# Kernel optimization log

Measured on AMD Instinct MI355X. Metric: run time of the kernel, lower is better.

The kernel has to match this reference:

```python
import jax, jax.numpy as jnp
import numpy as np

N = 40000
E = 640000
IN_C = 128
HID = 256
HEADS = 8


def _gat(x, W, att_src, att_dst, bias, src, dst, num_nodes, heads, concat):
    # x: [N, Fin], W: [Fin, heads*C], att_*: [heads, C], bias: [out_dim]
    xp = (x @ W).reshape(num_nodes, heads, -1)          # [N, H, C]
    a_s = jnp.sum(xp * att_src, axis=-1)                # [N, H]
    a_d = jnp.sum(xp * att_dst, axis=-1)                # [N, H]
    e = jax.nn.leaky_relu(a_s[src] + a_d[dst], 0.2)     # [E, H]
    # per-destination-node softmax over incoming edges (self-loops guarantee >=1)
    m = jax.ops.segment_max(e, dst, num_segments=num_nodes)
    m = jnp.where(jnp.isfinite(m), m, 0.0)
    ex = jnp.exp(e - m[dst])
    denom = jax.ops.segment_sum(ex, dst, num_segments=num_nodes)
    alpha = ex / (denom[dst] + 1e-16)                   # [E, H]
    out = jax.ops.segment_sum(xp[src] * alpha[..., None], dst, num_segments=num_nodes)  # [N,H,C]
    out = out.reshape(num_nodes, -1) if concat else out.mean(axis=1)
    return out + bias


def setup_inputs() -> dict:
    key = jax.random.key(0)
    ks = jax.random.split(key, 16)
    C = HID // HEADS
    s = 0.05
    return {
        "x": jax.random.normal(ks[0], (N, IN_C), jnp.float32),
        "edge_index": jax.random.randint(ks[1], (2, E), 0, N, jnp.int32),
        "W0": jax.random.normal(ks[2], (IN_C, HEADS * C), jnp.float32) * s,
        "att_s0": jax.random.normal(ks[3], (HEADS, C), jnp.float32) * s,
        "att_d0": jax.random.normal(ks[4], (HEADS, C), jnp.float32) * s,
        "b0": jnp.zeros((HID,), jnp.float32),
        # BatchNorm(256)
        "gamma0": jnp.ones((HID,), jnp.float32),
        "beta0": jnp.zeros((HID,), jnp.float32),
        # skip projection Linear(128 -> 256)
        "W_skip": jax.random.normal(ks[5], (IN_C, HID), jnp.float32) * s,
        "b_skip": jnp.zeros((HID,), jnp.float32),
        # last layer: GATConv(256 -> 256, heads=1, concat=False)
        "W1": jax.random.normal(ks[6], (HID, HID), jnp.float32) * s,
        "att_s1": jax.random.normal(ks[7], (1, HID), jnp.float32) * s,
        "att_d1": jax.random.normal(ks[8], (1, HID), jnp.float32) * s,
        "b1": jnp.zeros((HID,), jnp.float32),
    }


def reference(x, edge_index, W0, att_s0, att_d0, b0, gamma0, beta0,
              W_skip, b_skip, W1, att_s1, att_d1, b1):
    loops = jnp.arange(N, dtype=edge_index.dtype)
    src = jnp.concatenate([edge_index[0], loops])
    dst = jnp.concatenate([edge_index[1], loops])
    # conv 0 (heads=8, concat)
    h = _gat(x, W0, att_s0, att_d0, b0, src, dst, N, HEADS, True)
    # BatchNorm (training-style batch stats, biased variance, eps=1e-5)
    mu = h.mean(axis=0)
    var = h.var(axis=0)
    h = (h - mu) / jnp.sqrt(var + 1e-5) * gamma0 + beta0
    h = jax.nn.elu(h)
    # dropout is identity in eval mode
    # residual: shapes differ (128 vs 256) -> skip_proj(x_initial) + h at i==0
    h = h + (x @ W_skip + b_skip)
    # conv 1 (heads=1, concat=False -> mean over single head)
    out = _gat(h, W1, att_s1, att_d1, b1, src, dst, N, 1, False)
    return out
```

## Files before the change

kernel.cpp:

```cpp
#include <hip/hip_runtime.h>
#include <hip/hip_bf16.h>

#define NN 40000
#define EE 640000
#define ET 680000
#define MPAD 40064
#define LOG2E 1.4426950408889634f

typedef __attribute__((ext_vector_type(8))) short short8;
typedef __attribute__((ext_vector_type(4))) float f32x4;

__device__ __forceinline__ float bf2f(unsigned u) {
    return __uint_as_float(u << 16);
}
__device__ __forceinline__ unsigned short f2bf(float f) {
    unsigned u = __float_as_uint(f);
    return (unsigned short)((u + 0x7FFFu + ((u >> 16) & 1u)) >> 16);
}
__device__ __forceinline__ unsigned pack2(float lo, float hi) {
    return ((unsigned)f2bf(lo)) | (((unsigned)f2bf(hi)) << 16);
}
__device__ __forceinline__ void unpack2(unsigned u, float& lo, float& hi) {
    lo = __uint_as_float(u << 16);
    hi = __uint_as_float(u & 0xffff0000u);
}

__global__ __launch_bounds__(256) void conv_x(const float* __restrict__ x,
                                              unsigned short* __restrict__ xb)
{
    int i = blockIdx.x * 256 + threadIdx.x;
    if (i >= MPAD * 128 / 4) return;
    int row = (i * 4) >> 7;
    ushort4 o;
    if (row < NN) {
        float4 v = ((const float4*)x)[i];
        o.x = f2bf(v.x); o.y = f2bf(v.y); o.z = f2bf(v.z); o.w = f2bf(v.w);
    } else { o.x = o.y = o.z = o.w = 0; }
    ((ushort4*)xb)[i] = o;
}

__global__ __launch_bounds__(256) void conv_wt(const float* __restrict__ W,
                                               unsigned short* __restrict__ Wt, int K)
{
    int i = blockIdx.x * 256 + threadIdx.x;
    if (i >= K * 256) return;
    int c = i / K, k = i - c * K;
    Wt[i] = f2bf(W[(size_t)k * 256 + c]);
}

__global__ __launch_bounds__(256) void gemm_bf16(
    const unsigned short* __restrict__ A, const unsigned short* __restrict__ Btc,
    unsigned short* __restrict__ C0, unsigned short* __restrict__ C1, int K)
{
    __shared__ unsigned short As[128 * 64];
    int tid = threadIdx.x;
    int rb = blockIdx.x * 128, cb = blockIdx.y * 128;
    int lane = tid & 63, wid = tid >> 6;
    int wm = (wid >> 1) * 64, wn = (wid & 1) * 64;
    int lr = lane & 15, lk = lane >> 4;
    f32x4 acc[4][4] = {};
    for (int kb = 0; kb < K; kb += 64) {
        #pragma unroll
        for (int i = 0; i < 4; i++) {
            int flat = tid + i * 256;
            int r = flat >> 3, c8 = flat & 7;
            int4 v = *(const int4*)(A + (size_t)(rb + r) * K + kb + c8 * 8);
            *(int4*)(&As[r * 64 + ((c8 ^ (r & 7)) * 8)]) = v;
        }
        __syncthreads();
        #pragma unroll
        for (int kk = 0; kk < 2; kk++) {
            int kbase = kb + kk * 32 + lk * 8;
            short8 bfr[4], afr[4];
            #pragma unroll
            for (int n = 0; n < 4; n++)
                bfr[n] = *(const short8*)(Btc + (size_t)(cb + wn + n * 16 + lr) * K + kbase);
            #pragma unroll
            for (int m = 0; m < 4; m++) {
                int row = wm + m * 16 + lr;
                int kchunk = kk * 4 + lk;
                afr[m] = *(const short8*)(&As[row * 64 + ((kchunk ^ (row & 7)) * 8)]);
            }
            #pragma unroll
            for (int m = 0; m < 4; m++)
                #pragma unroll
                for (int n = 0; n < 4; n++)
                    acc[m][n] = __builtin_amdgcn_mfma_f32_16x16x32_bf16(afr[m], bfr[n], acc[m][n], 0, 0, 0);
        }
        __syncthreads();
    }
    unsigned short* C = (cb < 256) ? C0 : C1;
    int cbase = cb & 255;
    #pragma unroll
    for (int m = 0; m < 4; m++)
        #pragma unroll
        for (int n = 0; n < 4; n++) {
            int col = cbase + wn + n * 16 + lr;
            #pragma unroll
            for (int j = 0; j < 4; j++) {
                int row = rb + wm + m * 16 + lk * 4 + j;
                C[(size_t)row * 256 + col] = f2bf(acc[m][n][j]);
            }
        }
}

__global__ __launch_bounds__(256) void csr_count(const int* __restrict__ ei, int* __restrict__ deg)
{
    int e = blockIdx.x * blockDim.x + threadIdx.x;
    if (e >= ET) return;
    int d = (e < EE) ? ei[EE + e] : (e - EE);
    atomicAdd(&deg[d], 1);
}

__global__ __launch_bounds__(1024) void exscan(
    const int* __restrict__ deg, int* __restrict__ rowptr, int* __restrict__ cursor)
{
    __shared__ int wsum[16];
    __shared__ int carry_s;
    int tid = threadIdx.x, lane = tid & 63, wid = tid >> 6;
    if (tid == 0) carry_s = 0;
    __syncthreads();
    for (int base = 0; base < NN; base += 1024) {
        int i = base + tid;
        int v = (i < NN) ? deg[i] : 0;
        int sc = v;
        #pragma unroll
        for (int off = 1; off < 64; off <<= 1) {
            int t = __shfl_up(sc, off);
            if (lane >= off) sc += t;
        }
        if (lane == 63) wsum[wid] = sc;
        __syncthreads();
        if (wid == 0 && lane < 16) {
            int t = wsum[lane];
            #pragma unroll
            for (int off = 1; off < 16; off <<= 1) {
                int u = __shfl_up(t, off);
                if (lane >= off) t += u;
            }
            wsum[lane] = t;
        }
        __syncthreads();
        int carry = carry_s;
        int wpre = wid ? wsum[wid - 1] : 0;
        int excl = carry + wpre + sc - v;
        if (i < NN) { rowptr[i] = excl; cursor[i] = excl; }
        __syncthreads();
        if (tid == 0) carry_s = carry + wsum[15];
    }
    if (tid == 0) rowptr[NN] = carry_s;
}

__global__ __launch_bounds__(256) void csr_fill(
    const int* __restrict__ ei, int* __restrict__ cursor, int* __restrict__ adj)
{
    int e = blockIdx.x * blockDim.x + threadIdx.x;
    if (e >= ET) return;
    int s, d;
    if (e < EE) { s = ei[e]; d = ei[EE + e]; } else { s = d = e - EE; }
    int pos = atomicAdd(&cursor[d], 1);
    adj[pos] = s;
}

__global__ __launch_bounds__(256) void attn_node0(
    const unsigned short* __restrict__ xp, const float* __restrict__ att_s,
    const float* __restrict__ att_d, float* __restrict__ a_s, float* __restrict__ a_d)
{
    int t = blockIdx.x * 256 + threadIdx.x;
    if (t >= NN * 8) return;
    int n = t >> 3, h = t & 7;
    const unsigned short* p = xp + (size_t)n * 256 + h * 32;
    float s = 0.f, dd = 0.f;
    #pragma unroll
    for (int i0 = 0; i0 < 32; i0 += 8) {
        uint4 raw = *(const uint4*)(p + i0);
        unsigned vals[4] = {raw.x, raw.y, raw.z, raw.w};
        #pragma unroll
        for (int q = 0; q < 4; q++) {
            float lo, hi;
            unpack2(vals[q], lo, hi);
            s  += lo * att_s[h * 32 + i0 + q * 2] + hi * att_s[h * 32 + i0 + q * 2 + 1];
            dd += lo * att_d[h * 32 + i0 + q * 2] + hi * att_d[h * 32 + i0 + q * 2 + 1];
        }
    }
    a_s[t] = s * LOG2E; a_d[t] = dd * LOG2E;
}

__global__ __launch_bounds__(256) void attn_node1(
    const unsigned short* __restrict__ xp, const float* __restrict__ att_s,
    const float* __restrict__ att_d, float* __restrict__ a_s, float* __restrict__ a_d)
{
    int w = (blockIdx.x * 256 + threadIdx.x) >> 6;
    int lane = threadIdx.x & 63;
    if (w >= NN) return;
    ushort4 raw = ((const ushort4*)(xp + (size_t)w * 256))[lane];
    float4 a = ((const float4*)att_s)[lane];
    float4 b = ((const float4*)att_d)[lane];
    float v0 = bf2f(raw.x), v1 = bf2f(raw.y), v2 = bf2f(raw.z), v3 = bf2f(raw.w);
    float s  = v0 * a.x + v1 * a.y + v2 * a.z + v3 * a.w;
    float dd = v0 * b.x + v1 * b.y + v2 * b.z + v3 * b.w;
    #pragma unroll
    for (int off = 32; off; off >>= 1) {
        s  += __shfl_down(s, off);
        dd += __shfl_down(dd, off);
    }
    if (lane == 0) { a_s[w] = s * LOG2E; a_d[w] = dd * LOG2E; }
}

__global__ __launch_bounds__(256) void gather0(
    const int* __restrict__ adj, const int* __restrict__ rowptr,
    const unsigned short* __restrict__ xp, const float* __restrict__ a_s,
    const float* __restrict__ a_d, unsigned short* __restrict__ out0)
{
    int w = (blockIdx.x * 256 + threadIdx.x) >> 6;
    int lane = threadIdx.x & 63;
    if (w >= NN) return;
    int hl = lane & 31;
    int hw = lane >> 5;
    int h = hl >> 2;
    float ad = a_d[w * 8 + h];
    int p = rowptr[w], end = rowptr[w + 1];
    unsigned loff = (unsigned)hl * 16u;
    float a0=0,a1=0,a2=0,a3=0,a4=0,a5=0,a6=0,a7=0;
    float b0=0,b1=0,b2=0,b3=0,b4=0,b5=0,b6=0,b7=0;
    float den0 = 0.f, den1 = 0.f;
    for (; p + 4 <= end; p += 4) {
        int sA = adj[p + hw];
        int sB = adj[p + 2 + hw];
        float eA = a_s[sA * 8 + h] + ad;
        float eB = a_s[sB * 8 + h] + ad;
        float wA = __builtin_amdgcn_exp2f(fmaxf(eA, 0.2f * eA));
        float wB = __builtin_amdgcn_exp2f(fmaxf(eB, 0.2f * eB));
        uint4 rA = *(const uint4*)((const char*)xp + ((unsigned)sA * 512u + loff));
        uint4 rB = *(const uint4*)((const char*)xp + ((unsigned)sB * 512u + loff));
        den0 += wA; den1 += wB;
        float lo, hi;
        unpack2(rA.x, lo, hi); a0 += wA * lo; a1 += wA * hi;
        unpack2(rA.y, lo, hi); a2 += wA * lo; a3 += wA * hi;
        unpack2(rA.z, lo, hi); a4 += wA * lo; a5 += wA * hi;
        unpack2(rA.w, lo, hi); a6 += wA * lo; a7 += wA * hi;
        unpack2(rB.x, lo, hi); b0 += wB * lo; b1 += wB * hi;
        unpack2(rB.y, lo, hi); b2 += wB * lo; b3 += wB * hi;
        unpack2(rB.z, lo, hi); b4 += wB * lo; b5 += wB * hi;
        unpack2(rB.w, lo, hi); b6 += wB * lo; b7 += wB * hi;
    }
    for (; p + 2 <= end; p += 2) {
        int sA = adj[p + hw];
        float eA = a_s[sA * 8 + h] + ad;
        float wA = __builtin_amdgcn_exp2f(fmaxf(eA, 0.2f * eA));
        uint4 rA = *(const uint4*)((const char*)xp + ((unsigned)sA * 512u + loff));
        den0 += wA;
        float lo, hi;
        unpack2(rA.x, lo, hi); a0 += wA * lo; a1 += wA * hi;
        unpack2(rA.y, lo, hi); a2 += wA * lo; a3 += wA * hi;
        unpack2(rA.z, lo, hi); a4 += wA * lo; a5 += wA * hi;
        unpack2(rA.w, lo, hi); a6 += wA * lo; a7 += wA * hi;
    }
    if (p < end) {
        int sA = adj[p];
        float eA = a_s[sA * 8 + h] + ad;
        float wA = hw ? 0.f : __builtin_amdgcn_exp2f(fmaxf(eA, 0.2f * eA));
        uint4 rA = *(const uint4*)((const char*)xp + ((unsigned)sA * 512u + loff));
        den0 += wA;
        float lo, hi;
        unpack2(rA.x, lo, hi); a0 += wA * lo; a1 += wA * hi;
        unpack2(rA.y, lo, hi); a2 += wA * lo; a3 += wA * hi;
        unpack2(rA.z, lo, hi); a4 += wA * lo; a5 += wA * hi;
        unpack2(rA.w, lo, hi); a6 += wA * lo; a7 += wA * hi;
    }
    a0 += b0; a1 += b1; a2 += b2; a3 += b3;
    a4 += b4; a5 += b5; a6 += b6; a7 += b7;
    float den = den0 + den1;
    den += __shfl_xor(den, 32);
    a0 += __shfl_xor(a0, 32); a1 += __shfl_xor(a1, 32);
    a2 += __shfl_xor(a2, 32); a3 += __shfl_xor(a3, 32);
    a4 += __shfl_xor(a4, 32); a5 += __shfl_xor(a5, 32);
    a6 += __shfl_xor(a6, 32); a7 += __shfl_xor(a7, 32);
    if (hw == 0) {
        float inv = 1.f / (den + 1e-16f);
        uint4 o;
        o.x = pack2(a0 * inv, a1 * inv);
        o.y = pack2(a2 * inv, a3 * inv);
        o.z = pack2(a4 * inv, a5 * inv);
        o.w = pack2(a6 * inv, a7 * inv);
        *(uint4*)((char*)out0 + ((size_t)w * 512u + loff)) = o;
    }
}

__global__ __launch_bounds__(256) void bn_stats(
    const unsigned short* __restrict__ H, float* __restrict__ bnsum, float* __restrict__ bnsq)
{
    int c = threadIdx.x;
    int r0 = blockIdx.x * 64;
    float s = 0.f, sq = 0.f;
    for (int r = r0; r < r0 + 64; r++) {
        float v = bf2f(H[(size_t)r * 256 + c]);
        s += v; sq += v * v;
    }
    atomicAdd(&bnsum[c], s);
    atomicAdd(&bnsq[c], sq);
}

__global__ __launch_bounds__(256) void bn_coef(
    const float* __restrict__ bnsum, const float* __restrict__ bnsq,
    const float* __restrict__ gamma, const float* __restrict__ beta,
    float* __restrict__ scl, float* __restrict__ sft)
{
    int c = threadIdx.x;
    const float invN = 1.0f / (float)NN;
    float mu = bnsum[c] * invN;
    float var = bnsq[c] * invN - mu * mu;
    float s = rsqrtf(var + 1e-5f) * gamma[c];
    scl[c] = s;
    sft[c] = beta[c] - mu * s;
}

__global__ __launch_bounds__(256) void bn_elu(
    const unsigned short* __restrict__ out0, unsigned short* __restrict__ hb,
    const float* __restrict__ scl, const float* __restrict__ sft,
    const float* __restrict__ bskip)
{
    int i = blockIdx.x * 256 + threadIdx.x;
    if (i >= MPAD * 256 / 8) return;
    int col0 = (i * 8) & 255;
    uint4 hv = ((const uint4*)out0)[i];
    uint4 sv = ((const uint4*)hb)[i];
    float4 c0 = *(const float4*)(scl + col0);
    float4 c1 = *(const float4*)(scl + col0 + 4);
    float4 f0 = *(const float4*)(sft + col0);
    float4 f1 = *(const float4*)(sft + col0 + 4);
    float4 k0 = *(const float4*)(bskip + col0);
    float4 k1 = *(const float4*)(bskip + col0 + 4);
    float bn[8], sk[8];
    unpack2(hv.x, bn[0], bn[1]); unpack2(hv.y, bn[2], bn[3]);
    unpack2(hv.z, bn[4], bn[5]); unpack2(hv.w, bn[6], bn[7]);
    unpack2(sv.x, sk[0], sk[1]); unpack2(sv.y, sk[2], sk[3]);
    unpack2(sv.z, sk[4], sk[5]); unpack2(sv.w, sk[6], sk[7]);
    float cc[8] = {c0.x,c0.y,c0.z,c0.w,c1.x,c1.y,c1.z,c1.w};
    float ff[8] = {f0.x,f0.y,f0.z,f0.w,f1.x,f1.y,f1.z,f1.w};
    float kk[8] = {k0.x,k0.y,k0.z,k0.w,k1.x,k1.y,k1.z,k1.w};
    float r[8];
    #pragma unroll
    for (int q = 0; q < 8; q++) {
        float b = bn[q] * cc[q] + ff[q];
        float el = b > 0.f ? b : (__expf(b) - 1.f);
        r[q] = el + sk[q] + kk[q];
    }
    uint4 o;
    o.x = pack2(r[0], r[1]); o.y = pack2(r[2], r[3]);
    o.z = pack2(r[4], r[5]); o.w = pack2(r[6], r[7]);
    ((uint4*)hb)[i] = o;
}

__global__ __launch_bounds__(256) void gather1(
    const int* __restrict__ adj, const int* __restrict__ rowptr,
    const unsigned short* __restrict__ xp, const float* __restrict__ a_s,
    const float* __restrict__ a_d, const float* __restrict__ b1,
    float* __restrict__ out)
{
    int w = (blockIdx.x * 256 + threadIdx.x) >> 6;
    int lane = threadIdx.x & 63;
    if (w >= NN) return;
    int hl = lane & 31;
    int hw = lane >> 5;
    float ad = a_d[w];
    int p = rowptr[w], end = rowptr[w + 1];
    unsigned loff = (unsigned)hl * 16u;
    float a0=0,a1=0,a2=0,a3=0,a4=0,a5=0,a6=0,a7=0;
    float b0s=0,b1s=0,b2s=0,b3s=0,b4s=0,b5s=0,b6s=0,b7s=0;
    float den0 = 0.f, den1 = 0.f;
    for (; p + 4 <= end; p += 4) {
        int sA = adj[p + hw];
        int sB = adj[p + 2 + hw];
        float eA = a_s[sA] + ad;
        float eB = a_s[sB] + ad;
        float wA = __builtin_amdgcn_exp2f(fmaxf(eA, 0.2f * eA));
        float wB = __builtin_amdgcn_exp2f(fmaxf(eB, 0.2f * eB));
        uint4 rA = *(const uint4*)((const char*)xp + ((unsigned)sA * 512u + loff));
        uint4 rB = *(const uint4*)((const char*)xp + ((unsigned)sB * 512u + loff));
        den0 += wA; den1 += wB;
        float lo, hi;
        unpack2(rA.x, lo, hi); a0 += wA * lo; a1 += wA * hi;
        unpack2(rA.y, lo, hi); a2 += wA * lo; a3 += wA * hi;
        unpack2(rA.z, lo, hi); a4 += wA * lo; a5 += wA * hi;
        unpack2(rA.w, lo, hi); a6 += wA * lo; a7 += wA * hi;
        unpack2(rB.x, lo, hi); b0s += wB * lo; b1s += wB * hi;
        unpack2(rB.y, lo, hi); b2s += wB * lo; b3s += wB * hi;
        unpack2(rB.z, lo, hi); b4s += wB * lo; b5s += wB * hi;
        unpack2(rB.w, lo, hi); b6s += wB * lo; b7s += wB * hi;
    }
    for (; p + 2 <= end; p += 2) {
        int sA = adj[p + hw];
        float eA = a_s[sA] + ad;
        float wA = __builtin_amdgcn_exp2f(fmaxf(eA, 0.2f * eA));
        uint4 rA = *(const uint4*)((const char*)xp + ((unsigned)sA * 512u + loff));
        den0 += wA;
        float lo, hi;
        unpack2(rA.x, lo, hi); a0 += wA * lo; a1 += wA * hi;
        unpack2(rA.y, lo, hi); a2 += wA * lo; a3 += wA * hi;
        unpack2(rA.z, lo, hi); a4 += wA * lo; a5 += wA * hi;
        unpack2(rA.w, lo, hi); a6 += wA * lo; a7 += wA * hi;
    }
    if (p < end) {
        int sA = adj[p];
        float eA = a_s[sA] + ad;
        float wA = hw ? 0.f : __builtin_amdgcn_exp2f(fmaxf(eA, 0.2f * eA));
        uint4 rA = *(const uint4*)((const char*)xp + ((unsigned)sA * 512u + loff));
        den0 += wA;
        float lo, hi;
        unpack2(rA.x, lo, hi); a0 += wA * lo; a1 += wA * hi;
        unpack2(rA.y, lo, hi); a2 += wA * lo; a3 += wA * hi;
        unpack2(rA.z, lo, hi); a4 += wA * lo; a5 += wA * hi;
        unpack2(rA.w, lo, hi); a6 += wA * lo; a7 += wA * hi;
    }
    a0 += b0s; a1 += b1s; a2 += b2s; a3 += b3s;
    a4 += b4s; a5 += b5s; a6 += b6s; a7 += b7s;
    float den = den0 + den1;
    den += __shfl_xor(den, 32);
    a0 += __shfl_xor(a0, 32); a1 += __shfl_xor(a1, 32);
    a2 += __shfl_xor(a2, 32); a3 += __shfl_xor(a3, 32);
    a4 += __shfl_xor(a4, 32); a5 += __shfl_xor(a5, 32);
    a6 += __shfl_xor(a6, 32); a7 += __shfl_xor(a7, 32);
    if (hw == 0) {
        float inv = 1.f / (den + 1e-16f);
        const float* bb = b1 + hl * 8;
        float4 o0 = {a0 * inv + bb[0], a1 * inv + bb[1],
                     a2 * inv + bb[2], a3 * inv + bb[3]};
        float4 o1 = {a4 * inv + bb[4], a5 * inv + bb[5],
                     a6 * inv + bb[6], a7 * inv + bb[7]};
        float* orow = out + (size_t)w * 256 + hl * 8;
        *(float4*)(orow) = o0;
        *(float4*)(orow + 4) = o1;
    }
}

extern "C" void kernel_launch(void* const* d_in, const int* in_sizes, int n_in,
                              void* d_out, int out_size, void* d_ws, size_t ws_size,
                              hipStream_t stream)
{
    const float* x      = (const float*)d_in[0];
    const int*   ei     = (const int*)d_in[1];
    const float* W0     = (const float*)d_in[2];
    const float* att_s0 = (const float*)d_in[3];
    const float* att_d0 = (const float*)d_in[4];
    const float* gamma0 = (const float*)d_in[6];
    const float* beta0  = (const float*)d_in[7];
    const float* W_skip = (const float*)d_in[8];
    const float* b_skip = (const float*)d_in[9];
    const float* W1     = (const float*)d_in[10];
    const float* att_s1 = (const float*)d_in[11];
    const float* att_d1 = (const float*)d_in[12];
    const float* b1     = (const float*)d_in[13];
    float* out = (float*)d_out;

    char* p = (char*)d_ws;
    unsigned short* x_bf  = (unsigned short*)p; p += (size_t)MPAD * 128 * 2;
    unsigned short* xp_bf = (unsigned short*)p; p += (size_t)MPAD * 256 * 2;
    unsigned short* h_bf  = (unsigned short*)p; p += (size_t)MPAD * 256 * 2;
    unsigned short* out0b = (unsigned short*)p; p += (size_t)MPAD * 256 * 2;
    unsigned short* Wtc   = (unsigned short*)p; p += (size_t)512 * 128 * 2;
    unsigned short* W1t   = (unsigned short*)p; p += (size_t)256 * 256 * 2;
    float* a_s   = (float*)p; p += (size_t)NN * 8 * 4;
    float* a_d   = (float*)p; p += (size_t)NN * 8 * 4;
    float* bnsum = (float*)p; p += 256 * 4;
    float* bnsq  = (float*)p; p += 256 * 4;
    float* scl   = (float*)p; p += 256 * 4;
    float* sft   = (float*)p; p += 256 * 4;
    int* deg    = (int*)p; p += (size_t)NN * 4;
    int* rowptr = (int*)p; p += (size_t)(NN + 1) * 4;
    int* cursor = (int*)p; p += (size_t)NN * 4;
    int* adj    = (int*)p; p += (size_t)ET * 4;

    hipMemsetAsync(deg, 0, (size_t)NN * 4, stream);
    hipMemsetAsync(bnsum, 0, 512 * 4, stream);
    hipMemsetAsync(out0b + (size_t)NN * 256, 0, (size_t)(MPAD - NN) * 256 * 2, stream);

    conv_x<<<(MPAD * 128 / 4 + 255) / 256, 256, 0, stream>>>(x, x_bf);
    conv_wt<<<(128 * 256 + 255) / 256, 256, 0, stream>>>(W0, Wtc, 128);
    conv_wt<<<(128 * 256 + 255) / 256, 256, 0, stream>>>(W_skip, Wtc + 256 * 128, 128);
    conv_wt<<<(256 * 256 + 255) / 256, 256, 0, stream>>>(W1, W1t, 256);

    csr_count<<<(ET + 255) / 256, 256, 0, stream>>>(ei, deg);
    exscan<<<1, 1024, 0, stream>>>(deg, rowptr, cursor);
    csr_fill<<<(ET + 255) / 256, 256, 0, stream>>>(ei, cursor, adj);

    dim3 gg0(MPAD / 128, 4);
    gemm_bf16<<<gg0, 256, 0, stream>>>(x_bf, Wtc, xp_bf, h_bf, 128);
    attn_node0<<<(NN * 8 + 255) / 256, 256, 0, stream>>>(xp_bf, att_s0, att_d0, a_s, a_d);
    gather0<<<(NN * 64 + 255) / 256, 256, 0, stream>>>(adj, rowptr, xp_bf, a_s, a_d, out0b);

    bn_stats<<<NN / 64, 256, 0, stream>>>(out0b, bnsum, bnsq);
    bn_coef<<<1, 256, 0, stream>>>(bnsum, bnsq, gamma0, beta0, scl, sft);
    bn_elu<<<(MPAD * 256 / 8 + 255) / 256, 256, 0, stream>>>(out0b, h_bf, scl, sft, b_skip);

    dim3 gg1(MPAD / 128, 2);
    gemm_bf16<<<gg1, 256, 0, stream>>>(h_bf, W1t, xp_bf, xp_bf, 256);
    attn_node1<<<(NN * 64 + 255) / 256, 256, 0, stream>>>(xp_bf, att_s1, att_d1, a_s, a_d);
    gather1<<<(NN * 64 + 255) / 256, 256, 0, stream>>>(adj, rowptr, xp_bf, a_s, a_d, b1, out);
}
```

Before: 326.9 us.

## Fuse prep kernels, overlap CSR fill with GEMM0, fold layer-1 attention into BN

Merges the x/weight bf16 conversions, the degree count and a precomputed W1·att vector into one prep launch. CSR fill is co-scheduled with the first GEMM in a single grid. The BN coefficient computation is inlined into the BN/ELU kernel, which also computes layer-1 attention logits as h·(W1·att), so the separate attn_node1 pass over xp is removed. This cuts launch count and one full read of xp, but each thread now recomputes the BN coefficients per element, and the logits now come from fp32 h rather than the rounded bf16 projection, which slightly shifts the numerics.

```diff
diff --git a/kernel.cpp b/kernel.cpp
--- a/kernel.cpp
+++ b/kernel.cpp
@@ -7,6 +7,11 @@
 #define MPAD 40064
 #define LOG2E 1.4426950408889634f
 
+#define XN (MPAD * 128 / 4)
+#define WN 131072
+#define VN 512
+#define PREP_TOTAL (XN + WN + VN + ET)
+
 typedef __attribute__((ext_vector_type(8))) short short8;
 typedef __attribute__((ext_vector_type(4))) float f32x4;
 
@@ -25,32 +30,166 @@
     hi = __uint_as_float(u & 0xffff0000u);
 }
 
-__global__ __launch_bounds__(256) void conv_x(const float* __restrict__ x,
-                                              unsigned short* __restrict__ xb)
+__global__ __launch_bounds__(256) void prep(
+    const float* __restrict__ x, const float* __restrict__ W0,
+    const float* __restrict__ Ws, const float* __restrict__ W1,
+    const float* __restrict__ as1, const float* __restrict__ ad1,
+    const int* __restrict__ ei,
+    unsigned short* __restrict__ xb, unsigned short* __restrict__ Wtc,
+    unsigned short* __restrict__ W1t, float* __restrict__ v,
+    int* __restrict__ deg)
 {
     int i = blockIdx.x * 256 + threadIdx.x;
-    if (i >= MPAD * 128 / 4) return;
-    int row = (i * 4) >> 7;
-    ushort4 o;
-    if (row < NN) {
-        float4 v = ((const float4*)x)[i];
-        o.x = f2bf(v.x); o.y = f2bf(v.y); o.z = f2bf(v.z); o.w = f2bf(v.w);
-    } else { o.x = o.y = o.z = o.w = 0; }
-    ((ushort4*)xb)[i] = o;
-}
-
-__global__ __launch_bounds__(256) void conv_wt(const float* __restrict__ W,
-                                               unsigned short* __restrict__ Wt, int K)
-{
-    int i = blockIdx.x * 256 + threadIdx.x;
-    if (i >= K * 256) return;
-    int c = i / K, k = i - c * K;
-    Wt[i] = f2bf(W[(size_t)k * 256 + c]);
+    if (i < XN) {
+        int row = (i * 4) >> 7;
+        ushort4 o;
+        if (row < NN) {
+            float4 val = ((const float4*)x)[i];
+            o.x = f2bf(val.x); o.y = f2bf(val.y); o.z = f2bf(val.z); o.w = f2bf(val.w);
+        } else { o.x = o.y = o.z = o.w = 0; }
+        ((ushort4*)xb)[i] = o;
+    } else if (i < XN + WN) {
+        int j = i - XN;
+        if (j < 32768) {
+            int c = j >> 7, k = j & 127;
+            Wtc[j] = f2bf(W0[(size_t)k * 256 + c]);
+        } else if (j < 65536) {
+            int jj = j - 32768;
+            int c = jj >> 7, k = jj & 127;
+            Wtc[j] = f2bf(Ws[(size_t)k * 256 + c]);
+        } else {
+            int jj = j - 65536;
+            int c = jj >> 8, k = jj & 255;
+            W1t[jj] = f2bf(W1[(size_t)k * 256 + c]);
+        }
+    } else if (i < XN + WN + VN) {
+        int j = i - XN - WN;
+        int k = j >> 1, which = j & 1;
+        const float* att = which ? ad1 : as1;
+        float sum = 0.f;
+        for (int c = 0; c < 256; c++)
+            sum += W1[(size_t)k * 256 + c] * att[c];
+        v[j] = sum * LOG2E;
+    } else {
+        int e = i - XN - WN - VN;
+        if (e < ET) {
+            int d = (e < EE) ? ei[EE + e] : (e - EE);
+            atomicAdd(&deg[d], 1);
+        }
+    }
+}
+
+__global__ __launch_bounds__(1024) void exscan(
+    const int* __restrict__ deg, int* __restrict__ rowptr, int* __restrict__ cursor)
+{
+    __shared__ int wsum[16];
+    __shared__ int carry_s;
+    int tid = threadIdx.x, lane = tid & 63, wid = tid >> 6;
+    if (tid == 0) carry_s = 0;
+    __syncthreads();
+    for (int base = 0; base < NN; base += 1024) {
+        int i = base + tid;
+        int val = (i < NN) ? deg[i] : 0;
+        int sc = val;
+        #pragma unroll
+        for (int off = 1; off < 64; off <<= 1) {
+            int t = __shfl_up(sc, off);
+            if (lane >= off) sc += t;
+        }
+        if (lane == 63) wsum[wid] = sc;
+        __syncthreads();
+        if (wid == 0 && lane < 16) {
+            int t = wsum[lane];
+            #pragma unroll
+            for (int off = 1; off < 16; off <<= 1) {
+                int u = __shfl_up(t, off);
+                if (lane >= off) t += u;
+            }
+            wsum[lane] = t;
+        }
+        __syncthreads();
+        int carry = carry_s;
+        int wpre = wid ? wsum[wid - 1] : 0;
+        int excl = carry + wpre + sc - val;
+        if (i < NN) { rowptr[i] = excl; cursor[i] = excl; }
+        __syncthreads();
+        if (tid == 0) carry_s = carry + wsum[15];
+    }
+    if (tid == 0) rowptr[NN] = carry_s;
+}
+
+#define G0_BLOCKS 1252
+__global__ __launch_bounds__(256) void fill_gemm0(
+    const unsigned short* __restrict__ A, const unsigned short* __restrict__ Btc,
+    unsigned short* __restrict__ C0, unsigned short* __restrict__ C1,
+    const int* __restrict__ ei, int* __restrict__ cursor, int* __restrict__ adj)
+{
+    __shared__ unsigned short As[128 * 64];
+    int tid = threadIdx.x;
+    if (blockIdx.x >= G0_BLOCKS) {
+        int e = (blockIdx.x - G0_BLOCKS) * 256 + tid;
+        if (e < ET) {
+            int s, d;
+            if (e < EE) { s = ei[e]; d = ei[EE + e]; } else { s = d = e - EE; }
+            int pos = atomicAdd(&cursor[d], 1);
+            adj[pos] = s;
+        }
+        return;
+    }
+    const int K = 128;
+    int rb = (blockIdx.x >> 2) * 128, cb = (blockIdx.x & 3) * 128;
+    int lane = tid & 63, wid = tid >> 6;
+    int wm = (wid >> 1) * 64, wn = (wid & 1) * 64;
+    int lr = lane & 15, lk = lane >> 4;
+    f32x4 acc[4][4] = {};
+    for (int kb = 0; kb < K; kb += 64) {
+        #pragma unroll
+        for (int i = 0; i < 4; i++) {
+            int flat = tid + i * 256;
+            int r = flat >> 3, c8 = flat & 7;
+            int4 vv = *(const int4*)(A + (size_t)(rb + r) * K + kb + c8 * 8);
+            *(int4*)(&As[r * 64 + ((c8 ^ (r & 7)) * 8)]) = vv;
+        }
+        __syncthreads();
+        #pragma unroll
+        for (int kk = 0; kk < 2; kk++) {
+            int kbase = kb + kk * 32 + lk * 8;
+            short8 bfr[4], afr[4];
+            #pragma unroll
+            for (int n = 0; n < 4; n++)
+                bfr[n] = *(const short8*)(Btc + (size_t)(cb + wn + n * 16 + lr) * K + kbase);
+            #pragma unroll
+            for (int m = 0; m < 4; m++) {
+                int row = wm + m * 16 + lr;
+                int kchunk = kk * 4 + lk;
+                afr[m] = *(const short8*)(&As[row * 64 + ((kchunk ^ (row & 7)) * 8)]);
+            }
+            #pragma unroll
+            for (int m = 0; m < 4; m++)
+                #pragma unroll
+                for (int n = 0; n < 4; n++)
+                    acc[m][n] = __builtin_amdgcn_mfma_f32_16x16x32_bf16(afr[m], bfr[n], acc[m][n], 0, 0, 0);
+        }
+        __syncthreads();
+    }
+    unsigned short* C = (cb < 256) ? C0 : C1;
+    int cbase = cb & 255;
+    #pragma unroll
+    for (int m = 0; m < 4; m++)
+        #pragma unroll
+        for (int n = 0; n < 4; n++) {
+            int col = cbase + wn + n * 16 + lr;
+            #pragma unroll
+            for (int j = 0; j < 4; j++) {
+                int row = rb + wm + m * 16 + lk * 4 + j;
+                C[(size_t)row * 256 + col] = f2bf(acc[m][n][j]);
+            }
+        }
 }
 
 __global__ __launch_bounds__(256) void gemm_bf16(
     const unsigned short* __restrict__ A, const unsigned short* __restrict__ Btc,
-    unsigned short* __restrict__ C0, unsigned short* __restrict__ C1, int K)
+    unsigned short* __restrict__ C0, int K)
 {
     __shared__ unsigned short As[128 * 64];
     int tid = threadIdx.x;
@@ -64,8 +203,8 @@
         for (int i = 0; i < 4; i++) {
             int flat = tid + i * 256;
             int r = flat >> 3, c8 = flat & 7;
-            int4 v = *(const int4*)(A + (size_t)(rb + r) * K + kb + c8 * 8);
-            *(int4*)(&As[r * 64 + ((c8 ^ (r & 7)) * 8)]) = v;
+            int4 vv = *(const int4*)(A + (size_t)(rb + r) * K + kb + c8 * 8);
+            *(int4*)(&As[r * 64 + ((c8 ^ (r & 7)) * 8)]) = vv;
         }
         __syncthreads();
         #pragma unroll
@@ -89,77 +228,17 @@
         }
         __syncthreads();
     }
-    unsigned short* C = (cb < 256) ? C0 : C1;
-    int cbase = cb & 255;
     #pragma unroll
     for (int m = 0; m < 4; m++)
         #pragma unroll
         for (int n = 0; n < 4; n++) {
-            int col = cbase + wn + n * 16 + lr;
+            int col = cb + wn + n * 16 + lr;
             #pragma unroll
             for (int j = 0; j < 4; j++) {
                 int row = rb + wm + m * 16 + lk * 4 + j;
-                C[(size_t)row * 256 + col] = f2bf(acc[m][n][j]);
+                C0[(size_t)row * 256 + col] = f2bf(acc[m][n][j]);
             }
         }
-}
-
-__global__ __launch_bounds__(256) void csr_count(const int* __restrict__ ei, int* __restrict__ deg)
-{
-    int e = blockIdx.x * blockDim.x + threadIdx.x;
-    if (e >= ET) return;
-    int d = (e < EE) ? ei[EE + e] : (e - EE);
-    atomicAdd(&deg[d], 1);
-}
-
-__global__ __launch_bounds__(1024) void exscan(
-    const int* __restrict__ deg, int* __restrict__ rowptr, int* __restrict__ cursor)
-{
-    __shared__ int wsum[16];
-    __shared__ int carry_s;
-    int tid = threadIdx.x, lane = tid & 63, wid = tid >> 6;
-    if (tid == 0) carry_s = 0;
-    __syncthreads();
-    for (int base = 0; base < NN; base += 1024) {
-        int i = base + tid;
-        int v = (i < NN) ? deg[i] : 0;
-        int sc = v;
-        #pragma unroll
-        for (int off = 1; off < 64; off <<= 1) {
-            int t = __shfl_up(sc, off);
-            if (lane >= off) sc += t;
-        }
-        if (lane == 63) wsum[wid] = sc;
-        __syncthreads();
-        if (wid == 0 && lane < 16) {
-            int t = wsum[lane];
-            #pragma unroll
-            for (int off = 1; off < 16; off <<= 1) {
-                int u = __shfl_up(t, off);
-                if (lane >= off) t += u;
-            }
-            wsum[lane] = t;
-        }
-        __syncthreads();
-        int carry = carry_s;
-        int wpre = wid ? wsum[wid - 1] : 0;
-        int excl = carry + wpre + sc - v;
-        if (i < NN) { rowptr[i] = excl; cursor[i] = excl; }
-        __syncthreads();
-        if (tid == 0) carry_s = carry + wsum[15];
-    }
-    if (tid == 0) rowptr[NN] = carry_s;
-}
-
-__global__ __launch_bounds__(256) void csr_fill(
-    const int* __restrict__ ei, int* __restrict__ cursor, int* __restrict__ adj)
-{
-    int e = blockIdx.x * blockDim.x + threadIdx.x;
-    if (e >= ET) return;
-    int s, d;
-    if (e < EE) { s = ei[e]; d = ei[EE + e]; } else { s = d = e - EE; }
-    int pos = atomicAdd(&cursor[d], 1);
-    adj[pos] = s;
 }
 
 __global__ __launch_bounds__(256) void attn_node0(
@@ -184,27 +263,6 @@
         }
     }
     a_s[t] = s * LOG2E; a_d[t] = dd * LOG2E;
-}
-
-__global__ __launch_bounds__(256) void attn_node1(
-    const unsigned short* __restrict__ xp, const float* __restrict__ att_s,
-    const float* __restrict__ att_d, float* __restrict__ a_s, float* __restrict__ a_d)
-{
-    int w = (blockIdx.x * 256 + threadIdx.x) >> 6;
-    int lane = threadIdx.x & 63;
-    if (w >= NN) return;
-    ushort4 raw = ((const ushort4*)(xp + (size_t)w * 256))[lane];
-    float4 a = ((const float4*)att_s)[lane];
-    float4 b = ((const float4*)att_d)[lane];
-    float v0 = bf2f(raw.x), v1 = bf2f(raw.y), v2 = bf2f(raw.z), v3 = bf2f(raw.w);
-    float s  = v0 * a.x + v1 * a.y + v2 * a.z + v3 * a.w;
-    float dd = v0 * b.x + v1 * b.y + v2 * b.z + v3 * b.w;
-    #pragma unroll
-    for (int off = 32; off; off >>= 1) {
-        s  += __shfl_down(s, off);
-        dd += __shfl_down(dd, off);
-    }
-    if (lane == 0) { a_s[w] = s * LOG2E; a_d[w] = dd * LOG2E; }
 }
 
 __global__ __launch_bounds__(256) void gather0(
@@ -224,6 +282,7 @@
     float a0=0,a1=0,a2=0,a3=0,a4=0,a5=0,a6=0,a7=0;
     float b0=0,b1=0,b2=0,b3=0,b4=0,b5=0,b6=0,b7=0;
     float den0 = 0.f, den1 = 0.f;
+    float lo, hi;
     for (; p + 4 <= end; p += 4) {
         int sA = adj[p + hw];
         int sB = adj[p + 2 + hw];
@@ -234,7 +293,6 @@
         uint4 rA = *(const uint4*)((const char*)xp + ((unsigned)sA * 512u + loff));
         uint4 rB = *(const uint4*)((const char*)xp + ((unsigned)sB * 512u + loff));
         den0 += wA; den1 += wB;
-        float lo, hi;
         unpack2(rA.x, lo, hi); a0 += wA * lo; a1 += wA * hi;
         unpack2(rA.y, lo, hi); a2 += wA * lo; a3 += wA * hi;
         unpack2(rA.z, lo, hi); a4 += wA * lo; a5 += wA * hi;
@@ -250,7 +308,6 @@
         float wA = __builtin_amdgcn_exp2f(fmaxf(eA, 0.2f * eA));
         uint4 rA = *(const uint4*)((const char*)xp + ((unsigned)sA * 512u + loff));
         den0 += wA;
-        float lo, hi;
         unpack2(rA.x, lo, hi); a0 += wA * lo; a1 += wA * hi;
         unpack2(rA.y, lo, hi); a2 += wA * lo; a3 += wA * hi;
         unpack2(rA.z, lo, hi); a4 += wA * lo; a5 += wA * hi;
@@ -262,7 +319,6 @@
         float wA = hw ? 0.f : __builtin_amdgcn_exp2f(fmaxf(eA, 0.2f * eA));
         uint4 rA = *(const uint4*)((const char*)xp + ((unsigned)sA * 512u + loff));
         den0 += wA;
-        float lo, hi;
         unpack2(rA.x, lo, hi); a0 += wA * lo; a1 += wA * hi;
         unpack2(rA.y, lo, hi); a2 += wA * lo; a3 += wA * hi;
         unpack2(rA.z, lo, hi); a4 += wA * lo; a5 += wA * hi;
@@ -294,62 +350,60 @@
     int r0 = blockIdx.x * 64;
     float s = 0.f, sq = 0.f;
     for (int r = r0; r < r0 + 64; r++) {
-        float v = bf2f(H[(size_t)r * 256 + c]);
-        s += v; sq += v * v;
+        float val = bf2f(H[(size_t)r * 256 + c]);
+        s += val; sq += val * val;
     }
     atomicAdd(&bnsum[c], s);
     atomicAdd(&bnsq[c], sq);
 }
 
-__global__ __launch_bounds__(256) void bn_coef(
+__global__ __launch_bounds__(256) void bn_elu_attn(
+    const unsigned short* __restrict__ out0, unsigned short* __restrict__ hb,
     const float* __restrict__ bnsum, const float* __restrict__ bnsq,
     const float* __restrict__ gamma, const float* __restrict__ beta,
-    float* __restrict__ scl, float* __restrict__ sft)
-{
-    int c = threadIdx.x;
-    const float invN = 1.0f / (float)NN;
-    float mu = bnsum[c] * invN;
-    float var = bnsq[c] * invN - mu * mu;
-    float s = rsqrtf(var + 1e-5f) * gamma[c];
-    scl[c] = s;
-    sft[c] = beta[c] - mu * s;
-}
-
-__global__ __launch_bounds__(256) void bn_elu(
-    const unsigned short* __restrict__ out0, unsigned short* __restrict__ hb,
-    const float* __restrict__ scl, const float* __restrict__ sft,
-    const float* __restrict__ bskip)
+    const float* __restrict__ bskip, const float* __restrict__ v,
+    float* __restrict__ a_s, float* __restrict__ a_d)
 {
     int i = blockIdx.x * 256 + threadIdx.x;
-    if (i >= MPAD * 256 / 8) return;
+    if (i >= MPAD * 32) return;
     int col0 = (i * 8) & 255;
+    int row = i >> 5;
     uint4 hv = ((const uint4*)out0)[i];
     uint4 sv = ((const uint4*)hb)[i];
-    float4 c0 = *(const float4*)(scl + col0);
-    float4 c1 = *(const float4*)(scl + col0 + 4);
-    float4 f0 = *(const float4*)(sft + col0);
-    float4 f1 = *(const float4*)(sft + col0 + 4);
-    float4 k0 = *(const float4*)(bskip + col0);
-    float4 k1 = *(const float4*)(bskip + col0 + 4);
     float bn[8], sk[8];
     unpack2(hv.x, bn[0], bn[1]); unpack2(hv.y, bn[2], bn[3]);
     unpack2(hv.z, bn[4], bn[5]); unpack2(hv.w, bn[6], bn[7]);
     unpack2(sv.x, sk[0], sk[1]); unpack2(sv.y, sk[2], sk[3]);
     unpack2(sv.z, sk[4], sk[5]); unpack2(sv.w, sk[6], sk[7]);
-    float cc[8] = {c0.x,c0.y,c0.z,c0.w,c1.x,c1.y,c1.z,c1.w};
-    float ff[8] = {f0.x,f0.y,f0.z,f0.w,f1.x,f1.y,f1.z,f1.w};
-    float kk[8] = {k0.x,k0.y,k0.z,k0.w,k1.x,k1.y,k1.z,k1.w};
+    const float invN = 1.0f / (float)NN;
     float r[8];
+    float ps = 0.f, pd = 0.f;
     #pragma unroll
     for (int q = 0; q < 8; q++) {
-        float b = bn[q] * cc[q] + ff[q];
+        int c = col0 + q;
+        float mu = bnsum[c] * invN;
+        float var = bnsq[c] * invN - mu * mu;
+        float scl = rsqrtf(var + 1e-5f) * gamma[c];
+        float b = (bn[q] - mu) * scl + beta[c];
         float el = b > 0.f ? b : (__expf(b) - 1.f);
-        r[q] = el + sk[q] + kk[q];
+        r[q] = el + sk[q] + bskip[c];
+        float2 vv = *(const float2*)(v + c * 2);
+        ps += r[q] * vv.x;
+        pd += r[q] * vv.y;
     }
     uint4 o;
     o.x = pack2(r[0], r[1]); o.y = pack2(r[2], r[3]);
     o.z = pack2(r[4], r[5]); o.w = pack2(r[6], r[7]);
     ((uint4*)hb)[i] = o;
+    #pragma unroll
+    for (int off = 1; off < 32; off <<= 1) {
+        ps += __shfl_xor(ps, off);
+        pd += __shfl_xor(pd, off);
+    }
+    if ((threadIdx.x & 31) == 0 && row < NN) {
+        a_s[row] = ps;
+        a_d[row] = pd;
+    }
 }
 
 __global__ __launch_bounds__(256) void gather1(
@@ -369,6 +423,7 @@
     float a0=0,a1=0,a2=0,a3=0,a4=0,a5=0,a6=0,a7=0;
     float b0s=0,b1s=0,b2s=0,b3s=0,b4s=0,b5s=0,b6s=0,b7s=0;
     float den0 = 0.f, den1 = 0.f;
+    float lo, hi;
     for (; p + 4 <= end; p += 4) {
         int sA = adj[p + hw];
         int sB = adj[p + 2 + hw];
@@ -379,7 +434,6 @@
         uint4 rA = *(const uint4*)((const char*)xp + ((unsigned)sA * 512u + loff));
         uint4 rB = *(const uint4*)((const char*)xp + ((unsigned)sB * 512u + loff));
         den0 += wA; den1 += wB;
-        float lo, hi;
         unpack2(rA.x, lo, hi); a0 += wA * lo; a1 += wA * hi;
         unpack2(rA.y, lo, hi); a2 += wA * lo; a3 += wA * hi;
         unpack2(rA.z, lo, hi); a4 += wA * lo; a5 += wA * hi;
@@ -395,7 +449,6 @@
         float wA = __builtin_amdgcn_exp2f(fmaxf(eA, 0.2f * eA));
         uint4 rA = *(const uint4*)((const char*)xp + ((unsigned)sA * 512u + loff));
         den0 += wA;
-        float lo, hi;
         unpack2(rA.x, lo, hi); a0 += wA * lo; a1 += wA * hi;
         unpack2(rA.y, lo, hi); a2 += wA * lo; a3 += wA * hi;
         unpack2(rA.z, lo, hi); a4 += wA * lo; a5 += wA * hi;
@@ -407,7 +460,6 @@
         float wA = hw ? 0.f : __builtin_amdgcn_exp2f(fmaxf(eA, 0.2f * eA));
         uint4 rA = *(const uint4*)((const char*)xp + ((unsigned)sA * 512u + loff));
         den0 += wA;
-        float lo, hi;
         unpack2(rA.x, lo, hi); a0 += wA * lo; a1 += wA * hi;
         unpack2(rA.y, lo, hi); a2 += wA * lo; a3 += wA * hi;
         unpack2(rA.z, lo, hi); a4 += wA * lo; a5 += wA * hi;
@@ -460,41 +512,38 @@
     unsigned short* out0b = (unsigned short*)p; p += (size_t)MPAD * 256 * 2;
     unsigned short* Wtc   = (unsigned short*)p; p += (size_t)512 * 128 * 2;
     unsigned short* W1t   = (unsigned short*)p; p += (size_t)256 * 256 * 2;
+    float* v     = (float*)p; p += 512 * 4;
     float* a_s   = (float*)p; p += (size_t)NN * 8 * 4;
     float* a_d   = (float*)p; p += (size_t)NN * 8 * 4;
+    int*   deg   = (int*)p;   p += (size_t)NN * 4;
     float* bnsum = (float*)p; p += 256 * 4;
     float* bnsq  = (float*)p; p += 256 * 4;
-    float* scl   = (float*)p; p += 256 * 4;
-    float* sft   = (float*)p; p += 256 * 4;
-    int* deg    = (int*)p; p += (size_t)NN * 4;
     int* rowptr = (int*)p; p += (size_t)(NN + 1) * 4;
     int* cursor = (int*)p; p += (size_t)NN * 4;
     int* adj    = (int*)p; p += (size_t)ET * 4;
 
-    hipMemsetAsync(deg, 0, (size_t)NN * 4, stream);
-    hipMemsetAsync(bnsum, 0, 512 * 4, stream);
+    hipMemsetAsync(deg, 0, (size_t)(NN + 512) * 4, stream);
     hipMemsetAsync(out0b + (size_t)NN * 256, 0, (size_t)(MPAD - NN) * 256 * 2, stream);
 
-    conv_x<<<(MPAD * 128 / 4 + 255) / 256, 256, 0, stream>>>(x, x_bf);
-    conv_wt<<<(128 * 256 + 255) / 256, 256, 0, stream>>>(W0, Wtc, 128);
-    conv_wt<<<(128 * 256 + 255) / 256, 256, 0, stream>>>(W_skip, Wtc + 256 * 128, 128);
-    conv_wt<<<(256 * 256 + 255) / 256, 256, 0, stream>>>(W1, W1t, 256);
-
-    csr_count<<<(ET + 255) / 256, 256, 0, stream>>>(ei, deg);
+    prep<<<(PREP_TOTAL + 255) / 256, 256, 0, stream>>>(
+        x, W0, W_skip, W1, att_s1, att_d1, ei, x_bf, Wtc, W1t, v, deg);
+
     exscan<<<1, 1024, 0, stream>>>(deg, rowptr, cursor);
-    csr_fill<<<(ET + 255) / 256, 256, 0, stream>>>(ei, cursor, adj);
-
-    dim3 gg0(MPAD / 128, 4);
-    gemm_bf16<<<gg0, 256, 0, stream>>>(x_bf, Wtc, xp_bf, h_bf, 128);
+
+    fill_gemm0<<<G0_BLOCKS + (ET + 255) / 256, 256, 0, stream>>>(
+        x_bf, Wtc, xp_bf, h_bf, ei, cursor, adj);
+
     attn_node0<<<(NN * 8 + 255) / 256, 256, 0, stream>>>(xp_bf, att_s0, att_d0, a_s, a_d);
+
     gather0<<<(NN * 64 + 255) / 256, 256, 0, stream>>>(adj, rowptr, xp_bf, a_s, a_d, out0b);
 
     bn_stats<<<NN / 64, 256, 0, stream>>>(out0b, bnsum, bnsq);
-    bn_coef<<<1, 256, 0, stream>>>(bnsum, bnsq, gamma0, beta0, scl, sft);
-    bn_elu<<<(MPAD * 256 / 8 + 255) / 256, 256, 0, stream>>>(out0b, h_bf, scl, sft, b_skip);
+
+    bn_elu_attn<<<(MPAD * 32 + 255) / 256, 256, 0, stream>>>(
+        out0b, h_bf, bnsum, bnsq, gamma0, beta0, b_skip, v, a_s, a_d);
 
     dim3 gg1(MPAD / 128, 2);
-    gemm_bf16<<<gg1, 256, 0, stream>>>(h_bf, W1t, xp_bf, xp_bf, 256);
-    attn_node1<<<(NN * 64 + 255) / 256, 256, 0, stream>>>(xp_bf, att_s1, att_d1, a_s, a_d);
+    gemm_bf16<<<gg1, 256, 0, stream>>>(h_bf, W1t, xp_bf, 256);
+
     gather1<<<(NN * 64 + 255) / 256, 256, 0, stream>>>(adj, rowptr, xp_bf, a_s, a_d, b1, out);
 }
```

Result: faster. 316.7 us (-3.1%).
